# Optimization experiments

Hardware: AMD Instinct MI355X
Metric: run time of the kernel (lower is better)

Reference implementation:

```python
import jax, jax.numpy as jnp
import numpy as np

B, T = 128, 512
V, P, K = 10002, 500, 20
DC, DP, DT = 300, 100, 50
D = DC + DP + DT
H = 256


def setup_inputs() -> dict:
    key = jax.random.key(0)
    ks = jax.random.split(key, 21)
    s = lambda i, shape: jax.random.normal(ks[i], shape, jnp.float32) * 0.05
    return dict(
        x=jax.random.randint(ks[0], (B, T), 0, V),
        y=jax.random.randint(ks[1], (B, T), 0, K),
        pre_tags=jax.random.randint(ks[2], (B, T), 0, K),
        pinyin_tags=jax.random.randint(ks[3], (B, T), 0, P),
        mask=jnp.ones((B, T), bool),
        char_emb=s(4, (V, DC)),
        tag_emb=s(5, (K, DT)),
        pinyin_emb=s(6, (P, DP)),
        w_ih_f=s(7, (4 * H, D)), w_hh_f=s(8, (4 * H, H)), b_ih_f=s(9, (4 * H,)), b_hh_f=s(10, (4 * H,)),
        w_ih_b=s(11, (4 * H, D)), w_hh_b=s(12, (4 * H, H)), b_ih_b=s(13, (4 * H,)), b_hh_b=s(14, (4 * H,)),
        w_out=s(15, (K, 2 * H)), b_out=s(16, (K,)),
        start_trans=s(17, (K,)), end_trans=s(18, (K,)), trans=s(19, (K, K)),
    )


def _lstm_dir(xs, w_ih, w_hh, b_ih, b_hh, reverse):
    # xs: [T,B,D]; precompute input projection for all steps (one big GEMM)
    pre = jnp.einsum('tbd,gd->tbg', xs, w_ih) + b_ih + b_hh  # [T,B,4H]
    bsz = xs.shape[1]

    def step(carry, gx):
        h, c = carry
        g = gx + h @ w_hh.T
        i, f, gg, o = jnp.split(g, 4, axis=-1)  # torch gate order i,f,g,o
        c = jax.nn.sigmoid(f) * c + jax.nn.sigmoid(i) * jnp.tanh(gg)
        h = jax.nn.sigmoid(o) * jnp.tanh(c)
        return (h, c), h

    init = (jnp.zeros((bsz, H), xs.dtype), jnp.zeros((bsz, H), xs.dtype))
    _, hs = jax.lax.scan(step, init, pre, reverse=reverse)
    return hs  # [T,B,H]


def _emissions(x, pre_tags, pinyin_tags, char_emb, tag_emb, pinyin_emb,
               w_ih_f, w_hh_f, b_ih_f, b_hh_f, w_ih_b, w_hh_b, b_ih_b, b_hh_b,
               w_out, b_out):
    emb = jnp.concatenate([char_emb[x], pinyin_emb[pinyin_tags], tag_emb[pre_tags]], axis=2)  # [B,T,D]
    xs = emb.transpose(1, 0, 2)  # [T,B,D]
    hf = _lstm_dir(xs, w_ih_f, w_hh_f, b_ih_f, b_hh_f, reverse=False)
    hb = _lstm_dir(xs, w_ih_b, w_hh_b, b_ih_b, b_hh_b, reverse=True)
    h = jnp.concatenate([hf, hb], axis=-1)  # [T,B,2H]
    return jnp.einsum('tbh,kh->tbk', h, w_out) + b_out  # emissions [T,B,K]


def _crf_nll(em, tags, mask, start, trans, end):
    # em [T,B,K] (time-major), torchcrf forward with reduction='sum'
    tg = tags.T  # [T,B]
    mk = mask.T.astype(em.dtype)  # [T,B]
    # gold-path score
    first = start[tg[0]] + jnp.take_along_axis(em[0], tg[0][:, None], 1)[:, 0]

    def num_step(score, inputs):
        e_t, t_prev, t_cur, m = inputs
        s = trans[t_prev, t_cur] + jnp.take_along_axis(e_t, t_cur[:, None], 1)[:, 0]
        return score + s * m, None

    score, _ = jax.lax.scan(num_step, first, (em[1:], tg[:-1], tg[1:], mk[1:]))
    last_idx = (mask.sum(1) - 1).astype(jnp.int32)
    last_tag = jnp.take_along_axis(tags, last_idx[:, None].astype(tags.dtype), 1)[:, 0]
    score = score + end[last_tag]
    # partition function via forward algorithm
    alpha0 = start[None, :] + em[0]  # [B,K]

    def den_step(alpha, inputs):
        e_t, m = inputs
        nxt = jax.nn.logsumexp(alpha[:, :, None] + trans[None, :, :] + e_t[:, None, :], axis=1)
        return jnp.where(m[:, None] > 0, nxt, alpha), None

    alpha, _ = jax.lax.scan(den_step, alpha0, (em[1:], mk[1:]))
    logZ = jax.nn.logsumexp(alpha + end[None, :], axis=1)
    llh = jnp.sum(score - logZ)
    return -llh  # module returns -crf(...)


def reference(x, y, pre_tags, pinyin_tags, mask, char_emb, tag_emb, pinyin_emb,
              w_ih_f, w_hh_f, b_ih_f, b_hh_f, w_ih_b, w_hh_b, b_ih_b, b_hh_b,
              w_out, b_out, start_trans, end_trans, trans):
    em = _emissions(x, pre_tags, pinyin_tags, char_emb, tag_emb, pinyin_emb,
                    w_ih_f, w_hh_f, b_ih_f, b_hh_f, w_ih_b, w_hh_b, b_ih_b, b_hh_b,
                    w_out, b_out)
    return _crf_nll(em, y, mask, start_trans, trans, end_trans)
```

## Files before the change

kernel.cpp:

```cpp
#include <hip/hip_runtime.h>
#include <hip/hip_bf16.h>

typedef __attribute__((ext_vector_type(8))) short short8;
typedef __attribute__((ext_vector_type(4))) float float4v;
typedef __attribute__((ext_vector_type(4))) int int4v;

__device__ __forceinline__ float sigmoidf_(float x) {
  return __fdividef(1.f, 1.f + __expf(-x));
}
__device__ __forceinline__ float tanhf_(float x) {
  float e = __expf(2.f * x);
  return 1.f - __fdividef(2.f, e + 1.f);
}
__device__ __forceinline__ float bflo(unsigned int v) {
  return __uint_as_float(v << 16);
}
__device__ __forceinline__ float bfhi(unsigned int v) {
  return __uint_as_float(v & 0xffff0000u);
}
__device__ __forceinline__ void barrier_lgkm() {
  asm volatile("s_waitcnt lgkmcnt(0)\n\ts_barrier" ::: "memory");
}

__device__ __forceinline__ unsigned int pack4_(float4 v, float inv) {
  int b0 = (int)rintf(v.x * inv), b1 = (int)rintf(v.y * inv);
  int b2 = (int)rintf(v.z * inv), b3 = (int)rintf(v.w * inv);
  return (unsigned int)((b0 & 0xff) | ((b1 & 0xff) << 8) | ((b2 & 0xff) << 16) |
                        ((b3 & 0xff) << 24));
}

__device__ __forceinline__ int sel4_(int4v v, int rr) {
  int a = (rr & 1) ? v[1] : v[0];
  int b = (rr & 1) ? v[3] : v[2];
  return (rr & 2) ? b : a;
}

__global__ __launch_bounds__(256) void wquant_kernel(
    const float* __restrict__ whh_f, const float* __restrict__ whh_b,
    unsigned int* __restrict__ wq, float* __restrict__ wsc) {
  const int wave_g = blockIdx.x * 4 + (threadIdx.x >> 6);
  const int lane = threadIdx.x & 63;
  const int dir = wave_g >> 10, row = wave_g & 1023;
  const float* __restrict__ src = (dir ? whh_b : whh_f) + (size_t)row * 256;
  float4 v = ((const float4*)src)[lane];
  float mx = fmaxf(fmaxf(fabsf(v.x), fabsf(v.y)), fmaxf(fabsf(v.z), fabsf(v.w)));
#pragma unroll
  for (int k = 32; k >= 1; k >>= 1) mx = fmaxf(mx, __shfl_xor(mx, k, 64));
  float inv = (mx > 0.f) ? __fdividef(127.f, mx) : 0.f;
  wq[(size_t)wave_g * 64 + lane] = pack4_(v, inv);
  if (lane == 0) wsc[wave_g] = (mx > 0.f) ? (mx / (127.f * 127.f)) : 0.f;
}

__global__ __launch_bounds__(256) void proj_gemm(
    const float* __restrict__ A, int rowsA, int Kdim, int col_off,
    const float* __restrict__ wf, const float* __restrict__ wb,
    const float* __restrict__ bf1, const float* __restrict__ bf2,
    const float* __restrict__ bb1, const float* __restrict__ bb2,
    __hip_bfloat16* __restrict__ out, int add_bias) {
  __shared__ __align__(16) __hip_bfloat16 As[128][40];
  __shared__ __align__(16) __hip_bfloat16 Bs[256][40];
  const int tid = threadIdx.x;
  const int m0 = blockIdx.x * 128, n0 = blockIdx.y * 256;
  const int lane = tid & 63, wave = tid >> 6;
  const int quad = lane >> 4, lm = lane & 15;
  float4v acc[2][16] = {};
  const int ksteps = (Kdim + 31) >> 5;
  const int r2 = tid >> 1, cbase = (tid & 1) << 4;
  const int rb = tid >> 4, cb = (tid & 15) * 2;
  for (int ks = 0; ks < ksteps; ++ks) {
    const int k0 = ks << 5;
#pragma unroll
    for (int e2 = 0; e2 < 8; ++e2) {
      int kk = k0 + cbase + 2 * e2;
      float b0 = 0.f, b1 = 0.f;
      if (m0 + r2 < rowsA && kk < Kdim) {
        float2 v = *(const float2*)(A + (size_t)(m0 + r2) * Kdim + kk);
        b0 = v.x;
        b1 = v.y;
      }
      As[r2][cbase + 2 * e2] = __float2bfloat16(b0);
      As[r2][cbase + 2 * e2 + 1] = __float2bfloat16(b1);
    }
#pragma unroll
    for (int j = 0; j < 16; ++j) {
      int n = n0 + rb + 16 * j;
      const float* __restrict__ wrow =
          (n < 1024) ? (wf + n * 450 + col_off) : (wb + (n - 1024) * 450 + col_off);
      int kk = k0 + cb;
      float b0 = 0.f, b1 = 0.f;
      if (kk < Kdim) {
        float2 v = *(const float2*)(wrow + kk);
        b0 = v.x;
        b1 = v.y;
      }
      Bs[rb + 16 * j][cb] = __float2bfloat16(b0);
      Bs[rb + 16 * j][cb + 1] = __float2bfloat16(b1);
    }
    __syncthreads();
    short8 af0 = *(const short8*)(&As[wave * 32 + lm][quad * 8]);
    short8 af1 = *(const short8*)(&As[wave * 32 + 16 + lm][quad * 8]);
#pragma unroll
    for (int t = 0; t < 16; ++t) {
      short8 bf = *(const short8*)(&Bs[t * 16 + lm][quad * 8]);
      acc[0][t] = __builtin_amdgcn_mfma_f32_16x16x32_bf16(af0, bf, acc[0][t], 0, 0, 0);
      acc[1][t] = __builtin_amdgcn_mfma_f32_16x16x32_bf16(af1, bf, acc[1][t], 0, 0, 0);
    }
    __syncthreads();
  }
#pragma unroll
  for (int mg = 0; mg < 2; ++mg) {
#pragma unroll
    for (int t = 0; t < 16; ++t) {
#pragma unroll
      for (int rr = 0; rr < 4; ++rr) {
        int m = m0 + wave * 32 + mg * 16 + quad * 4 + rr;
        int col = n0 + t * 16 + lm;
        if (m < rowsA) {
          float v = acc[mg][t][rr];
          if (add_bias)
            v += (col < 1024) ? (bf1[col] + bf2[col]) : (bb1[col - 1024] + bb2[col - 1024]);
          int dir = col >> 10, rq = col & 1023;
          int gate = rq >> 8, u = rq & 255;
          out[m * 2048 + dir * 1024 + u * 4 + gate] = __float2bfloat16(v);
        }
      }
    }
  }
}

__global__ __launch_bounds__(256) void pgsum_kernel(
    const __hip_bfloat16* __restrict__ pin, const __hip_bfloat16* __restrict__ tag,
    __hip_bfloat16* __restrict__ pg) {
  const int r = blockIdx.x;
  const int p = r / 20, g = r - p * 20;
  const int i = threadIdx.x;
  const short8 va = *(const short8*)(pin + (size_t)p * 2048 + i * 8);
  const short8 vb = *(const short8*)(tag + (size_t)g * 2048 + i * 8);
  short8 vo;
#pragma unroll
  for (int j = 0; j < 8; ++j) {
    float a = __uint_as_float(((unsigned)(unsigned short)va[j]) << 16);
    float b = __uint_as_float(((unsigned)(unsigned short)vb[j]) << 16);
    __hip_bfloat16 o = __float2bfloat16(a + b);
    vo[j] = *(short*)&o;
  }
  *(short8*)(pg + (size_t)r * 2048 + i * 8) = vo;
}

template <int USE_PG>
__global__ __launch_bounds__(512, 2) void lstm_kernel(
    const unsigned int* __restrict__ wq, const float* __restrict__ wsc,
    const int* __restrict__ x, const int* __restrict__ ptags, const int* __restrict__ gtags,
    const char* __restrict__ char_proj, const char* __restrict__ pin_proj,
    const char* __restrict__ tag_proj, const char* __restrict__ pg_proj,
    __hip_bfloat16* __restrict__ h_out) {
  extern __shared__ __align__(16) char smem[];
  __hip_bfloat16* hist = (__hip_bfloat16*)smem;
  char* hqb = smem + 16384;

  const int tid = threadIdx.x;
  const int w = tid >> 6, lane = tid & 63;
  const int quad = lane >> 4, lm = lane & 15;
  const int sel = lm >> 1;
  const int mt = sel >> 2, rr = sel & 3;
  const int unit = w * 32 + mt * 16 + quad * 4 + rr;
  const int chain = blockIdx.x;
  const int dir = chain >> 7;
  const int b = chain & 127;
  const int boff = b * 512;

  if (tid < 34) ((uint4*)hqb)[tid] = make_uint4(0, 0, 0, 0);

  const unsigned int* __restrict__ wqd = wq + (size_t)dir * 65536;
  int4v Wf[4][2][4];
#pragma unroll
  for (int g = 0; g < 4; ++g)
#pragma unroll
    for (int m = 0; m < 2; ++m) {
      const int row = g * 256 + w * 32 + m * 16 + lm;
#pragma unroll
      for (int kt = 0; kt < 4; ++kt)
        Wf[g][m][kt] = *(const int4v*)(wqd + row * 64 + kt * 16 + quad * 4);
    }
  float sc4[4];
#pragma unroll
  for (int g = 0; g < 4; ++g) sc4[g] = wsc[dir * 1024 + g * 256 + unit];
  __syncthreads();

  const int pre_off = dir * 2048 + unit * 8;
  float cst = 0.f;

  int t_cur = dir ? 511 : 0;
  int t_nxt = dir ? 510 : 1;
  uint2 vc, vp, vg;
  int xn, pgn, pn, gn;
  {
    int xc = x[boff + t_cur], pc = ptags[boff + t_cur], gc = gtags[boff + t_cur];
    vc = *(const uint2*)(char_proj + (size_t)xc * 4096 + pre_off);
    if (USE_PG) {
      vp = *(const uint2*)(pg_proj + (size_t)(pc * 20 + gc) * 4096 + pre_off);
    } else {
      vp = *(const uint2*)(pin_proj + (size_t)pc * 4096 + pre_off);
      vg = *(const uint2*)(tag_proj + (size_t)gc * 4096 + pre_off);
    }
    xn = x[boff + t_nxt];
    pn = ptags[boff + t_nxt];
    gn = gtags[boff + t_nxt];
    if (USE_PG) pgn = pn * 20 + gn;
  }

  int4v Bv[4];
#pragma unroll
  for (int kt = 0; kt < 4; ++kt)
    Bv[kt] = *(const int4v*)(hqb + kt * 64 + quad * 16);

  for (int s = 0; s < 512; ++s) {
    const int nxt = (s & 1) ^ 1;
    const uint2 cv = vc, pv = vp, gv = vg;
    const int t_fut = dir ? (t_nxt > 0 ? t_nxt - 1 : 0) : (t_nxt < 511 ? t_nxt + 1 : 511);
    vc = *(const uint2*)(char_proj + (size_t)xn * 4096 + pre_off);
    if (USE_PG) {
      vp = *(const uint2*)(pg_proj + (size_t)pgn * 4096 + pre_off);
    } else {
      vp = *(const uint2*)(pin_proj + (size_t)pn * 4096 + pre_off);
      vg = *(const uint2*)(tag_proj + (size_t)gn * 4096 + pre_off);
    }
    xn = x[boff + t_fut];
    pn = ptags[boff + t_fut];
    gn = gtags[boff + t_fut];
    if (USE_PG) pgn = pn * 20 + gn;

    int4v acc[4][2] = {};
    __builtin_amdgcn_s_setprio(1);
#pragma unroll
    for (int kt = 0; kt < 4; ++kt) {
#pragma unroll
      for (int g = 0; g < 4; ++g)
#pragma unroll
        for (int m = 0; m < 2; ++m)
          acc[g][m] = __builtin_amdgcn_mfma_i32_16x16x64_i8(Wf[g][m][kt], Bv[kt], acc[g][m], 0, 0, 0);
    }
    __builtin_amdgcn_s_setprio(0);

    int ai = mt ? sel4_(acc[0][1], rr) : sel4_(acc[0][0], rr);
    int af = mt ? sel4_(acc[1][1], rr) : sel4_(acc[1][0], rr);
    int ag = mt ? sel4_(acc[2][1], rr) : sel4_(acc[2][0], rr);
    int ao = mt ? sel4_(acc[3][1], rr) : sel4_(acc[3][0], rr);
    float gi, gf, gg, go;
    if (USE_PG) {
      gi = bflo(cv.x) + bflo(pv.x) + (float)ai * sc4[0];
      gf = bfhi(cv.x) + bfhi(pv.x) + (float)af * sc4[1];
      gg = bflo(cv.y) + bflo(pv.y) + (float)ag * sc4[2];
      go = bfhi(cv.y) + bfhi(pv.y) + (float)ao * sc4[3];
    } else {
      gi = bflo(cv.x) + bflo(pv.x) + bflo(gv.x) + (float)ai * sc4[0];
      gf = bfhi(cv.x) + bfhi(pv.x) + bfhi(gv.x) + (float)af * sc4[1];
      gg = bflo(cv.y) + bflo(pv.y) + bflo(gv.y) + (float)ag * sc4[2];
      go = bfhi(cv.y) + bfhi(pv.y) + bfhi(gv.y) + (float)ao * sc4[3];
    }
    cst = sigmoidf_(gf) * cst + sigmoidf_(gi) * tanhf_(gg);
    float hval = sigmoidf_(go) * tanhf_(cst);
    if (!(lm & 1)) {
      ((signed char*)hqb)[nxt * 272 + unit] = (signed char)(int)rintf(hval * 127.f);
    }
    barrier_lgkm();
#pragma unroll
    for (int kt = 0; kt < 4; ++kt)
      Bv[kt] = *(const int4v*)(hqb + nxt * 272 + kt * 64 + quad * 16);
    if (!(lm & 1)) hist[(s & 31) * 256 + unit] = __float2bfloat16(hval);
    if ((s & 15) == 15) {
      barrier_lgkm();
      const int slotBase = (s & 31) & ~15;
      const int sBase = s - 15;
      const int row = tid >> 5;
      const int col16 = tid & 31;
      uint4 v = *(const uint4*)((const char*)hist + (slotBase + row) * 512 + col16 * 16);
      int step_r = sBase + row;
      int t_r = dir ? (511 - step_r) : step_r;
      *(uint4*)((char*)h_out + ((size_t)(chain * 512 + t_r) * 256) * 2 + col16 * 16) = v;
    }
    t_cur = t_nxt;
    t_nxt = t_fut;
  }
}

__global__ __launch_bounds__(256) void emis_kernel(
    const __hip_bfloat16* __restrict__ h_glob, const float* __restrict__ w_out,
    const float* __restrict__ b_out, float* __restrict__ em) {
  __shared__ __align__(16) __hip_bfloat16 As[64][40];
  __shared__ __align__(16) __hip_bfloat16 Bs[32][40];
  const int tid = threadIdx.x;
  const int n0 = blockIdx.x * 64;
  const int lane = tid & 63, wave = tid >> 6, quad = lane >> 4, lm = lane & 15;
  float4v acc[2] = {};
  const int r = tid >> 2, c0 = (tid & 3) << 3;
  const int rb = tid >> 3, cb = (tid & 7) << 2;
  for (int ks = 0; ks < 16; ++ks) {
    const int j0 = ks * 32;
    const int dirk = j0 >> 8, jin = j0 & 255;
    const int n = n0 + r, bb = n >> 9, tt = n & 511;
    const uint4* src =
        (const uint4*)(h_glob + ((size_t)(dirk * 128 + bb) * 512 + tt) * 256 + jin + c0);
    *(uint4*)(&As[r][c0]) = *src;
#pragma unroll
    for (int e = 0; e < 4; ++e) {
      float v = (rb < 20) ? w_out[rb * 512 + j0 + cb + e] : 0.f;
      Bs[rb][cb + e] = __float2bfloat16(v);
    }
    __syncthreads();
    short8 af = *(const short8*)(&As[wave * 16 + lm][quad * 8]);
#pragma unroll
    for (int t2 = 0; t2 < 2; ++t2) {
      short8 bf = *(const short8*)(&Bs[t2 * 16 + lm][quad * 8]);
      acc[t2] = __builtin_amdgcn_mfma_f32_16x16x32_bf16(af, bf, acc[t2], 0, 0, 0);
    }
    __syncthreads();
  }
#pragma unroll
  for (int t2 = 0; t2 < 2; ++t2) {
#pragma unroll
    for (int rr = 0; rr < 4; ++rr) {
      int col = t2 * 16 + lm;
      if (col < 20) {
        int n = n0 + wave * 16 + quad * 4 + rr;
        em[(size_t)n * 20 + col] = acc[t2][rr] + b_out[col];
      }
    }
  }
}

__global__ __launch_bounds__(64) void crf_kernel(
    const float* __restrict__ em, const int* __restrict__ y,
    const float* __restrict__ start_trans, const float* __restrict__ end_trans,
    const float* __restrict__ trans, float* __restrict__ partials) {
  const int b = blockIdx.x;
  const int lane = threadIdx.x;
  const int jj = lane < 20 ? lane : 19;
  const bool act = lane < 20;
  const float* __restrict__ emb = em + (size_t)b * 512 * 20;
  const int* __restrict__ yb = y + b * 512;

  float s_part = 0.f;
#pragma unroll
  for (int i = 0; i < 8; ++i) {
    int t = lane + 64 * i;
    int yc = yb[t];
    float v = emb[t * 20 + yc];
    v += (t == 0) ? start_trans[yc] : trans[yb[t - 1] * 20 + yc];
    s_part += v;
  }
#pragma unroll
  for (int k = 32; k >= 1; k >>= 1) s_part += __shfl_xor(s_part, k, 64);
  float score = s_part + end_trans[yb[511]];

  float ET[20];
#pragma unroll
  for (int i = 0; i < 20; ++i) ET[i] = __expf(trans[i * 20 + jj]);
  float alpha = act ? (start_trans[jj] + emb[jj]) : -1e30f;
  float P = alpha;
#pragma unroll
  for (int k = 32; k >= 1; k >>= 1) P = fmaxf(P, __shfl_xor(P, k, 64));

  float eC = emb[1 * 20 + jj];
  float eN = emb[2 * 20 + jj];
  for (int t = 1; t < 512; ++t) {
    if ((t & 15) == 0) {
      P = alpha;
#pragma unroll
      for (int k = 32; k >= 1; k >>= 1) P = fmaxf(P, __shfl_xor(P, k, 64));
    }
    float ex = __expf(alpha - P);
    float s0 = 0.f, s1 = 0.f;
#pragma unroll
    for (int i = 0; i < 20; i += 2) {
      float e0 = __int_as_float(__builtin_amdgcn_readlane(__float_as_int(ex), i));
      float e1 = __int_as_float(__builtin_amdgcn_readlane(__float_as_int(ex), i + 1));
      s0 = fmaf(e0, ET[i], s0);
      s1 = fmaf(e1, ET[i + 1], s1);
    }
    int tf = t + 2 < 512 ? t + 2 : 511;
    float eF = emb[tf * 20 + jj];
    if (act) alpha = P + __logf(s0 + s1) + eC;
    eC = eN;
    eN = eF;
  }
  float v = act ? (alpha + end_trans[jj]) : -1e30f;
  float Pz = v;
#pragma unroll
  for (int k = 32; k >= 1; k >>= 1) Pz = fmaxf(Pz, __shfl_xor(Pz, k, 64));
  float e2 = __expf(v - Pz);
#pragma unroll
  for (int k = 32; k >= 1; k >>= 1) e2 += __shfl_xor(e2, k, 64);
  float logZ = Pz + __logf(e2);
  if (lane == 0) partials[b] = logZ - score;
}

__global__ __launch_bounds__(128) void reduce_kernel(const float* __restrict__ partials,
                                                     float* __restrict__ out) {
  const int tid = threadIdx.x;
  float v = partials[tid];
#pragma unroll
  for (int k = 32; k >= 1; k >>= 1) v += __shfl_xor(v, k, 64);
  __shared__ float tmp[2];
  if ((tid & 63) == 0) tmp[tid >> 6] = v;
  __syncthreads();
  if (tid == 0) out[0] = tmp[0] + tmp[1];
}

extern "C" void kernel_launch(void* const* d_in, const int* in_sizes, int n_in,
                              void* d_out, int out_size, void* d_ws, size_t ws_size,
                              hipStream_t stream) {
  const int* x = (const int*)d_in[0];
  const int* y = (const int*)d_in[1];
  const int* pre_tags = (const int*)d_in[2];
  const int* pinyin_tags = (const int*)d_in[3];
  const float* char_emb = (const float*)d_in[5];
  const float* tag_emb = (const float*)d_in[6];
  const float* pinyin_emb = (const float*)d_in[7];
  const float* w_ih_f = (const float*)d_in[8];
  const float* w_hh_f = (const float*)d_in[9];
  const float* b_ih_f = (const float*)d_in[10];
  const float* b_hh_f = (const float*)d_in[11];
  const float* w_ih_b = (const float*)d_in[12];
  const float* w_hh_b = (const float*)d_in[13];
  const float* b_ih_b = (const float*)d_in[14];
  const float* b_hh_b = (const float*)d_in[15];
  const float* w_out = (const float*)d_in[16];
  const float* b_out = (const float*)d_in[17];
  const float* start_trans = (const float*)d_in[18];
  const float* end_trans = (const float*)d_in[19];
  const float* trans = (const float*)d_in[20];

  char* ws = (char*)d_ws;
  __hip_bfloat16* char_proj = (__hip_bfloat16*)(ws);
  __hip_bfloat16* pin_proj = (__hip_bfloat16*)(ws + 40968192);
  __hip_bfloat16* tag_proj = (__hip_bfloat16*)(ws + 43016192);
  __hip_bfloat16* h_glob = (__hip_bfloat16*)(ws + 43098112);
  float* em = (float*)(ws + 110206976);
  float* partials = (float*)(ws + 115449856);
  unsigned int* wq = (unsigned int*)(ws + 110206976);
  float* wsc = (float*)(ws + 110206976 + 524288);
  __hip_bfloat16* pg_proj = (__hip_bfloat16*)(ws + 115450368);
  const bool use_pg = ws_size >= (size_t)115450368 + 40960000;

  wquant_kernel<<<512, 256, 0, stream>>>(w_hh_f, w_hh_b, wq, wsc);

  proj_gemm<<<dim3(79, 8), 256, 0, stream>>>(char_emb, 10002, 300, 0, w_ih_f, w_ih_b,
                                             nullptr, nullptr, nullptr, nullptr, char_proj, 0);
  proj_gemm<<<dim3(4, 8), 256, 0, stream>>>(pinyin_emb, 500, 100, 300, w_ih_f, w_ih_b,
                                            nullptr, nullptr, nullptr, nullptr, pin_proj, 0);
  proj_gemm<<<dim3(1, 8), 256, 0, stream>>>(tag_emb, 20, 50, 400, w_ih_f, w_ih_b,
                                            b_ih_f, b_hh_f, b_ih_b, b_hh_b, tag_proj, 1);
  if (use_pg) pgsum_kernel<<<10000, 256, 0, stream>>>(pin_proj, tag_proj, pg_proj);

  const int lstm_lds = 16928;
  if (use_pg) {
    hipFuncSetAttribute((const void*)lstm_kernel<1>, hipFuncAttributeMaxDynamicSharedMemorySize,
                        lstm_lds);
    lstm_kernel<1><<<256, 512, lstm_lds, stream>>>(wq, wsc, x, pinyin_tags, pre_tags,
                                                   (const char*)char_proj, (const char*)pin_proj,
                                                   (const char*)tag_proj, (const char*)pg_proj,
                                                   h_glob);
  } else {
    hipFuncSetAttribute((const void*)lstm_kernel<0>, hipFuncAttributeMaxDynamicSharedMemorySize,
                        lstm_lds);
    lstm_kernel<0><<<256, 512, lstm_lds, stream>>>(wq, wsc, x, pinyin_tags, pre_tags,
                                                   (const char*)char_proj, (const char*)pin_proj,
                                                   (const char*)tag_proj, (const char*)pg_proj,
                                                   h_glob);
  }

  emis_kernel<<<1024, 256, 0, stream>>>(h_glob, w_out, b_out, em);
  crf_kernel<<<128, 64, 0, stream>>>(em, y, start_trans, end_trans, trans, partials);
  reduce_kernel<<<1, 128, 0, stream>>>(partials, (float*)d_out);
}
```

Baseline: 954.4 us.

## Split LSTM recurrence across 16 waves and write h directly to global

The recurrent LSTM kernel now runs with 1024 threads per chain (16 waves), each wave owning 16 hidden units instead of 32. This halves the per-wave MFMA chain per step and halves the weight registers held per wave. The LDS history buffer and the periodic block flush of h are removed: each unit stores its bf16 h straight to global memory every step. Half of the next step's B operand loads are also deferred to the start of the following iteration so they overlap the gate-input fetches. The cost is a wider barrier across 16 waves each step and many small scattered global stores.

```diff
diff --git a/kernel.cpp b/kernel.cpp
--- a/kernel.cpp
+++ b/kernel.cpp
@@ -148,22 +148,20 @@
 }
 
 template <int USE_PG>
-__global__ __launch_bounds__(512, 2) void lstm_kernel(
+__global__ __launch_bounds__(1024, 4) void lstm_kernel(
     const unsigned int* __restrict__ wq, const float* __restrict__ wsc,
     const int* __restrict__ x, const int* __restrict__ ptags, const int* __restrict__ gtags,
     const char* __restrict__ char_proj, const char* __restrict__ pin_proj,
     const char* __restrict__ tag_proj, const char* __restrict__ pg_proj,
     __hip_bfloat16* __restrict__ h_out) {
   extern __shared__ __align__(16) char smem[];
-  __hip_bfloat16* hist = (__hip_bfloat16*)smem;
-  char* hqb = smem + 16384;
+  char* hqb = smem;
 
   const int tid = threadIdx.x;
   const int w = tid >> 6, lane = tid & 63;
   const int quad = lane >> 4, lm = lane & 15;
-  const int sel = lm >> 1;
-  const int mt = sel >> 2, rr = sel & 3;
-  const int unit = w * 32 + mt * 16 + quad * 4 + rr;
+  const int rr = lm & 3;
+  const int unit = w * 16 + quad * 4 + rr;
   const int chain = blockIdx.x;
   const int dir = chain >> 7;
   const int b = chain & 127;
@@ -172,16 +170,14 @@
   if (tid < 34) ((uint4*)hqb)[tid] = make_uint4(0, 0, 0, 0);
 
   const unsigned int* __restrict__ wqd = wq + (size_t)dir * 65536;
-  int4v Wf[4][2][4];
-#pragma unroll
-  for (int g = 0; g < 4; ++g)
-#pragma unroll
-    for (int m = 0; m < 2; ++m) {
-      const int row = g * 256 + w * 32 + m * 16 + lm;
-#pragma unroll
-      for (int kt = 0; kt < 4; ++kt)
-        Wf[g][m][kt] = *(const int4v*)(wqd + row * 64 + kt * 16 + quad * 4);
-    }
+  int4v Wf[4][4];
+#pragma unroll
+  for (int g = 0; g < 4; ++g) {
+    const int row = g * 256 + w * 16 + lm;
+#pragma unroll
+    for (int kt = 0; kt < 4; ++kt)
+      Wf[g][kt] = *(const int4v*)(wqd + row * 64 + kt * 16 + quad * 4);
+  }
   float sc4[4];
 #pragma unroll
   for (int g = 0; g < 4; ++g) sc4[g] = wsc[dir * 1024 + g * 256 + unit];
@@ -209,13 +205,15 @@
     if (USE_PG) pgn = pn * 20 + gn;
   }
 
-  int4v Bv[4];
-#pragma unroll
-  for (int kt = 0; kt < 4; ++kt)
-    Bv[kt] = *(const int4v*)(hqb + kt * 64 + quad * 16);
+  int4v Bv0, Bv1, Bv2, Bv3;
+  Bv0 = *(const int4v*)(hqb + 0 * 64 + quad * 16);
+  Bv1 = *(const int4v*)(hqb + 1 * 64 + quad * 16);
 
   for (int s = 0; s < 512; ++s) {
-    const int nxt = (s & 1) ^ 1;
+    const int cur = s & 1, nxt = cur ^ 1;
+    Bv2 = *(const int4v*)(hqb + cur * 272 + 2 * 64 + quad * 16);
+    Bv3 = *(const int4v*)(hqb + cur * 272 + 3 * 64 + quad * 16);
+
     const uint2 cv = vc, pv = vp, gv = vg;
     const int t_fut = dir ? (t_nxt > 0 ? t_nxt - 1 : 0) : (t_nxt < 511 ? t_nxt + 1 : 511);
     vc = *(const uint2*)(char_proj + (size_t)xn * 4096 + pre_off);
@@ -230,22 +228,26 @@
     gn = gtags[boff + t_fut];
     if (USE_PG) pgn = pn * 20 + gn;
 
-    int4v acc[4][2] = {};
+    int4v acc[4] = {};
     __builtin_amdgcn_s_setprio(1);
 #pragma unroll
-    for (int kt = 0; kt < 4; ++kt) {
-#pragma unroll
-      for (int g = 0; g < 4; ++g)
-#pragma unroll
-        for (int m = 0; m < 2; ++m)
-          acc[g][m] = __builtin_amdgcn_mfma_i32_16x16x64_i8(Wf[g][m][kt], Bv[kt], acc[g][m], 0, 0, 0);
-    }
+    for (int g = 0; g < 4; ++g)
+      acc[g] = __builtin_amdgcn_mfma_i32_16x16x64_i8(Wf[g][0], Bv0, acc[g], 0, 0, 0);
+#pragma unroll
+    for (int g = 0; g < 4; ++g)
+      acc[g] = __builtin_amdgcn_mfma_i32_16x16x64_i8(Wf[g][1], Bv1, acc[g], 0, 0, 0);
+#pragma unroll
+    for (int g = 0; g < 4; ++g)
+      acc[g] = __builtin_amdgcn_mfma_i32_16x16x64_i8(Wf[g][2], Bv2, acc[g], 0, 0, 0);
+#pragma unroll
+    for (int g = 0; g < 4; ++g)
+      acc[g] = __builtin_amdgcn_mfma_i32_16x16x64_i8(Wf[g][3], Bv3, acc[g], 0, 0, 0);
     __builtin_amdgcn_s_setprio(0);
 
-    int ai = mt ? sel4_(acc[0][1], rr) : sel4_(acc[0][0], rr);
-    int af = mt ? sel4_(acc[1][1], rr) : sel4_(acc[1][0], rr);
-    int ag = mt ? sel4_(acc[2][1], rr) : sel4_(acc[2][0], rr);
-    int ao = mt ? sel4_(acc[3][1], rr) : sel4_(acc[3][0], rr);
+    int ai = sel4_(acc[0], rr);
+    int af = sel4_(acc[1], rr);
+    int ag = sel4_(acc[2], rr);
+    int ao = sel4_(acc[3], rr);
     float gi, gf, gg, go;
     if (USE_PG) {
       gi = bflo(cv.x) + bflo(pv.x) + (float)ai * sc4[0];
@@ -260,25 +262,13 @@
     }
     cst = sigmoidf_(gf) * cst + sigmoidf_(gi) * tanhf_(gg);
     float hval = sigmoidf_(go) * tanhf_(cst);
-    if (!(lm & 1)) {
+    if (lm < 4) {
       ((signed char*)hqb)[nxt * 272 + unit] = (signed char)(int)rintf(hval * 127.f);
+      h_out[(size_t)(chain * 512 + t_cur) * 256 + unit] = __float2bfloat16(hval);
     }
     barrier_lgkm();
-#pragma unroll
-    for (int kt = 0; kt < 4; ++kt)
-      Bv[kt] = *(const int4v*)(hqb + nxt * 272 + kt * 64 + quad * 16);
-    if (!(lm & 1)) hist[(s & 31) * 256 + unit] = __float2bfloat16(hval);
-    if ((s & 15) == 15) {
-      barrier_lgkm();
-      const int slotBase = (s & 31) & ~15;
-      const int sBase = s - 15;
-      const int row = tid >> 5;
-      const int col16 = tid & 31;
-      uint4 v = *(const uint4*)((const char*)hist + (slotBase + row) * 512 + col16 * 16);
-      int step_r = sBase + row;
-      int t_r = dir ? (511 - step_r) : step_r;
-      *(uint4*)((char*)h_out + ((size_t)(chain * 512 + t_r) * 256) * 2 + col16 * 16) = v;
-    }
+    Bv0 = *(const int4v*)(hqb + nxt * 272 + 0 * 64 + quad * 16);
+    Bv1 = *(const int4v*)(hqb + nxt * 272 + 1 * 64 + quad * 16);
     t_cur = t_nxt;
     t_nxt = t_fut;
   }
@@ -453,21 +443,21 @@
                                             b_ih_f, b_hh_f, b_ih_b, b_hh_b, tag_proj, 1);
   if (use_pg) pgsum_kernel<<<10000, 256, 0, stream>>>(pin_proj, tag_proj, pg_proj);
 
-  const int lstm_lds = 16928;
+  const int lstm_lds = 1024;
   if (use_pg) {
     hipFuncSetAttribute((const void*)lstm_kernel<1>, hipFuncAttributeMaxDynamicSharedMemorySize,
                         lstm_lds);
-    lstm_kernel<1><<<256, 512, lstm_lds, stream>>>(wq, wsc, x, pinyin_tags, pre_tags,
-                                                   (const char*)char_proj, (const char*)pin_proj,
-                                                   (const char*)tag_proj, (const char*)pg_proj,
-                                                   h_glob);
+    lstm_kernel<1><<<256, 1024, lstm_lds, stream>>>(wq, wsc, x, pinyin_tags, pre_tags,
+                                                    (const char*)char_proj, (const char*)pin_proj,
+                                                    (const char*)tag_proj, (const char*)pg_proj,
+                                                    h_glob);
   } else {
     hipFuncSetAttribute((const void*)lstm_kernel<0>, hipFuncAttributeMaxDynamicSharedMemorySize,
                         lstm_lds);
-    lstm_kernel<0><<<256, 512, lstm_lds, stream>>>(wq, wsc, x, pinyin_tags, pre_tags,
-                                                   (const char*)char_proj, (const char*)pin_proj,
-                                                   (const char*)tag_proj, (const char*)pg_proj,
-                                                   h_glob);
+    lstm_kernel<0><<<256, 1024, lstm_lds, stream>>>(wq, wsc, x, pinyin_tags, pre_tags,
+                                                    (const char*)char_proj, (const char*)pin_proj,
+                                                    (const char*)tag_proj, (const char*)pg_proj,
+                                                    h_glob);
   }
 
   emis_kernel<<<1024, 256, 0, stream>>>(h_glob, w_out, b_out, em);
```

After: 1.071 ms. 12.2% more time.
